# Kernel optimization log

Measured on AMD Instinct MI355X. Metric: run time of the kernel, lower is better.

Reference implementation:

```python
import jax, jax.numpy as jnp
import numpy as np

EPS_NORM = 1e-12   # torch F.normalize eps
GN_EPS = 1e-5      # GroupNorm eps
FACTOR = 5
NUM_HEADS = 8
NEG_SLOPE = 0.01   # LeakyReLU default


def _l2norm(x, axis):
    n = jnp.sqrt(jnp.sum(x * x, axis=axis, keepdims=True))
    return x / jnp.maximum(n, EPS_NORM)


def setup_inputs() -> dict:
    key = jax.random.key(0)
    B, C, H, W, D = 2, 256, 16, 16, 16
    N = H * W * D
    sample_k = FACTOR * int(np.ceil(np.log(N)))  # 45
    ks = jax.random.split(key, 8)
    s = 0.02
    return {
        "x": jax.random.normal(ks[0], (B, C, H, W, D), jnp.float32),
        "W_qkvv": jax.random.normal(ks[1], (C, 4 * C), jnp.float32) * s,
        "W_out": jax.random.normal(ks[2], (C, C), jnp.float32) * s,
        "b_out": jnp.zeros((C,), jnp.float32),
        "W_out2": jax.random.normal(ks[3], (C, C), jnp.float32) * s,
        "b_out2": jnp.zeros((C,), jnp.float32),
        "gamma1": 0.1 * jnp.ones((C,), jnp.float32),
        "conv_w": jax.random.normal(ks[4], (C, C, 3, 3, 3), jnp.float32) * s,
        "gn_w": jnp.ones((C,), jnp.float32),
        "gn_b": jnp.zeros((C,), jnp.float32),
        "index_sample": jax.random.randint(ks[5], (N, sample_k), 0, N),
    }


def reference(x, W_qkvv, W_out, b_out, W_out2, b_out2, gamma1, conv_w, gn_w, gn_b, index_sample):
    B, C, H, Wd, D = x.shape
    N = H * Wd * D
    nh = NUM_HEADS
    dh = C // nh
    xs = x.reshape(B, C, N).transpose(0, 2, 1)                    # [B,N,C]
    qkvv = (xs @ W_qkvv).reshape(B, N, 4, nh, dh).transpose(2, 0, 3, 1, 4)  # [4,B,nh,N,dh]
    q, k, v_ca, v_sa = qkvv[0], qkvv[1], qkvv[2], qkvv[3]
    q = _l2norm(q, axis=-2)   # normalize over sequence dim (dim=-2 in torch)
    k = _l2norm(k, axis=-2)

    u = FACTOR * int(np.ceil(np.log(N)))
    # --- ProbSparse _prob_QK ---
    K_sample = k[:, :, index_sample, :]                            # [B,nh,N,sk,dh]
    QK_sample = jnp.einsum('bhle,bhlse->bhls', q, K_sample)        # [B,nh,N,sk]
    M = QK_sample.max(-1) - QK_sample.sum(-1) / N                  # sparsity measure
    _, M_top = jax.lax.top_k(M, u)                                 # [B,nh,u]
    b_idx = jnp.arange(B)[:, None, None]
    h_idx = jnp.arange(nh)[None, :, None]
    Q_red = q[b_idx, h_idx, M_top]                                 # [B,nh,u,dh]
    scores = jnp.einsum('bhud,bhld->bhul', Q_red, k)               # [B,nh,u,N]

    # --- spatial (ProbSparse) context ---
    ctx = jnp.broadcast_to(v_sa.mean(axis=-2, keepdims=True), v_sa.shape)  # [B,nh,N,dh]
    attn_sa = jax.nn.softmax(scores, axis=-1)
    upd = jnp.einsum('bhul,bhld->bhud', attn_sa, v_sa)             # [B,nh,u,dh]
    ctx = ctx.at[b_idx, h_idx, M_top].set(upd)

    # --- channel attention (on transposed q,k,v: [B,nh,dh,N]) ---
    qt = q.transpose(0, 1, 3, 2)
    kt = k.transpose(0, 1, 3, 2)
    vt = v_ca.transpose(0, 1, 3, 2)
    attn_ca = jax.nn.softmax(jnp.einsum('bhdn,bhen->bhde', qt, kt), axis=-1)  # [B,nh,dh,dh]
    x_ca = jnp.einsum('bhde,bhen->bhdn', attn_ca, vt).transpose(0, 3, 1, 2).reshape(B, N, C)
    x_sa = ctx.transpose(0, 3, 1, 2).reshape(B, N, C)              # matches source permute
    x_sa = x_sa @ W_out + b_out                                    # dead branch (source discards)
    x_ca = x_ca @ W_out2 + b_out2
    epa = x_ca  # source: x = x_SA + x_CA; x = x_CA  -> only CA branch survives

    attn = xs + gamma1 * epa                                       # [B,N,C]
    attn = attn.reshape(B, H, Wd, D, C).transpose(0, 4, 1, 2, 3)   # [B,C,H,W,D]

    # conv8: Dropout3d (eval=id) -> Conv3d(3x3x3, no bias) -> GroupNorm(1 group)
    y = jax.lax.conv_general_dilated(attn, conv_w, (1, 1, 1), [(1, 1)] * 3,
                                     dimension_numbers=('NCDHW', 'OIDHW', 'NCDHW'))
    mu = y.mean(axis=(1, 2, 3, 4), keepdims=True)
    var = y.var(axis=(1, 2, 3, 4), keepdims=True)
    y = (y - mu) / jnp.sqrt(var + GN_EPS)
    y = y * gn_w[None, :, None, None, None] + gn_b[None, :, None, None, None]
    y = y + attn
    return jnp.where(y >= 0, y, NEG_SLOPE * y)
```

## Files before the change

### kernel.cpp

```cpp
#include <hip/hip_runtime.h>
#include <hip/hip_bf16.h>
#include <stdint.h>


#define B_ 2
#define C_ 256
#define N_ 4096
#define NH 8
#define PADV 5832
#define CN  (C_*N_)
#define BCN (B_*CN)

typedef unsigned short u16;
typedef unsigned int   u32;

using frag16 = __attribute__((ext_vector_type(8))) short;
using f32x4  = __attribute__((ext_vector_type(4))) float;

__device__ __forceinline__ u16 f2bf(float f) {
    u32 u = __float_as_uint(f);
    u += 0x7fff + ((u >> 16) & 1);
    return (u16)(u >> 16);
}
__device__ __forceinline__ float bb(u16 h) { return __uint_as_float((u32)h << 16); }
__device__ __forceinline__ void gld16(const void* g, void* l) {
    __builtin_amdgcn_global_load_lds((const __attribute__((address_space(1))) u32*)g,
                                     (__attribute__((address_space(3))) u32*)l, 16, 0, 0);
}
__device__ __forceinline__ int padrow(int n) {
    int z = n >> 8, y = (n >> 4) & 15, x = n & 15;
    return (z + 1) * 324 + (y + 1) * 18 + (x + 1);
}

#define OFF_TB    0
#define OFF_SP    3145728
#define OFF_XCAB  3276800
#define OFF_PK    0
#define OFF_ATTB  6291456
#define OFF_ATTP  7340032
#define OFF_WT2   8833024
#define OFF_W2B   9717760
#define OFF_WQB   9750528
#define OFF_XT    9848832
#define OFF_RED   10897408
 
__global__ __launch_bounds__(256) void k_prep(const float* __restrict__ CW, const float* __restrict__ W2,
                                              const float* __restrict__ Wq, const float* __restrict__ X,
                                              u16* __restrict__ WT2, u16* __restrict__ W2B,
                                              u16* __restrict__ Wqb, u16* __restrict__ XT,
                                              u32* __restrict__ APz) {
    __shared__ float ts[32][33];
    int blk = blockIdx.x, tid = threadIdx.x;
    if (blk < 6912) {
        int o = blk * 256 + tid;
        int ci = o & 255, co = (o >> 8) & 255, t = o >> 16;
        WT2[o] = f2bf(CW[((size_t)co * 256 + ci) * 27 + t]);
    } else if (blk < 6976) {
        int bi = blk - 6912; int c0 = (bi & 7) * 32, p0 = (bi >> 3) * 32;
        int tx = tid & 31, ty = tid >> 5;
#pragma unroll
        for (int i = 0; i < 4; ++i) ts[ty + i * 8][tx] = W2[(size_t)(p0 + ty + i * 8) * 256 + c0 + tx];
        __syncthreads();
#pragma unroll
        for (int i = 0; i < 4; ++i) W2B[(size_t)(c0 + ty + i * 8) * 256 + p0 + tx] = f2bf(ts[tx][ty + i * 8]);
    } else if (blk < 7744) {
        int o = (blk - 6976) * 256 + tid;
        int c = o & 255, j = o >> 8;
        Wqb[o] = f2bf(Wq[(size_t)c * 1024 + j]);
    } else if (blk < 9792) {
        int idx = blk - 7744;
        int n0 = (idx & 127) * 32, c0 = ((idx >> 7) & 7) * 32, b = idx >> 10;
        int tx = tid & 31, ty = tid >> 5;
        const float* Xb = X + (size_t)b * CN;
#pragma unroll
        for (int i = 0; i < 4; ++i) ts[ty + i * 8][tx] = Xb[(size_t)(c0 + ty + i * 8) * N_ + n0 + tx];
        __syncthreads();
        u16* Xo = XT + (size_t)b * N_ * C_;
#pragma unroll
        for (int i = 0; i < 4; ++i) Xo[(size_t)(n0 + ty + i * 8) * C_ + c0 + tx] = f2bf(ts[tx][ty + i * 8]);
    } else {
        APz[(size_t)(blk - 9792) * 256 + tid] = 0;
    }
}

__global__ __launch_bounds__(256) void k_qkv_mfma(const u16* __restrict__ Wqb, const u16* __restrict__ XT,
                                                  u16* __restrict__ Tb) {
    __shared__ __align__(16) u16 As[2][8192], Bs[2][8192];
    int n0 = blockIdx.x * 128, j0 = blockIdx.y * 128, b = blockIdx.z;
    int tid = threadIdx.x, lane = tid & 63, w = tid >> 6;
    int wm = w & 1, wn = w >> 1, qm = lane >> 4, lm = lane & 15;
    int srow = lane >> 3;
    int sperm = (((lane & 7) ^ srow) << 3);
    const u16* aB = Wqb + ((size_t)(j0 + w * 32 + srow) << 8) + sperm;
    const u16* bB = XT + ((size_t)(b * N_ + n0 + w * 32 + srow) << 8) + sperm;
    int rdp = ((lm & 7) << 3);
    f32x4 acc[4][4] = {};
    auto stg = [&](int p, int kc) {
#pragma unroll
        for (int i = 0; i < 4; ++i) {
            gld16(aB + i * 2048 + kc * 64, &As[p][w * 2048 + i * 512]);
            gld16(bB + i * 2048 + kc * 64, &Bs[p][w * 2048 + i * 512]);
        }
    };
    stg(0, 0);
#pragma unroll
    for (int kt = 0; kt < 4; ++kt) {
        int p = kt & 1;
        __syncthreads();
        if (kt < 3) stg(p ^ 1, kt + 1);
#pragma unroll
        for (int c2 = 0; c2 < 2; ++c2) {
            frag16 af[4], bf[4];
#pragma unroll
            for (int i = 0; i < 4; ++i)
                af[i] = *(const frag16*)&As[p][(wm * 64 + i * 16 + lm) * 64 + ((((c2 * 4 + qm) << 3) ^ rdp))];
#pragma unroll
            for (int j = 0; j < 4; ++j)
                bf[j] = *(const frag16*)&Bs[p][(wn * 64 + j * 16 + lm) * 64 + ((((c2 * 4 + qm) << 3) ^ rdp))];
#pragma unroll
            for (int i = 0; i < 4; ++i)
#pragma unroll
                for (int j = 0; j < 4; ++j)
                    acc[i][j] = __builtin_amdgcn_mfma_f32_16x16x32_bf16(af[i], bf[j], acc[i][j], 0, 0, 0);
        }
    }
    u16* To = Tb + ((size_t)b * 768 + j0 + wm * 64) * N_ + n0 + wn * 64;
#pragma unroll
    for (int i = 0; i < 4; ++i)
#pragma unroll
        for (int j = 0; j < 4; ++j)
#pragma unroll
            for (int r = 0; r < 4; ++r)
                To[(size_t)(i * 16 + qm * 4 + r) * N_ + j * 16 + lm] = f2bf(acc[i][j][r]);
}

__global__ __launch_bounds__(256) void k_l2norm(u16* __restrict__ Tb) {
    int bj = blockIdx.x; int b = bj >> 9, j = bj & 511;
    u16* row = Tb + ((size_t)b * 768 + j) * N_;
    float s = 0.f;
    for (int u = threadIdx.x * 8; u < N_; u += 2048) {
        uint4 vv = *(const uint4*)(row + u);
        const u16* h = (const u16*)&vv;
#pragma unroll
        for (int i = 0; i < 8; ++i) { float f = bb(h[i]); s += f * f; }
    }
#pragma unroll
    for (int off = 32; off; off >>= 1) s += __shfl_down(s, off);
    __shared__ float rs_[4]; __shared__ float rtot;
    int lane = threadIdx.x & 63, wv = threadIdx.x >> 6;
    if (!lane) rs_[wv] = s;
    __syncthreads();
    if (threadIdx.x == 0) rtot = 1.0f / fmaxf(sqrtf(rs_[0] + rs_[1] + rs_[2] + rs_[3]), 1e-12f);
    __syncthreads();
    float rn = rtot;
    for (int u = threadIdx.x * 8; u < N_; u += 2048) {
        uint4 vv = *(const uint4*)(row + u);
        u16* h = (u16*)&vv;
#pragma unroll
        for (int i = 0; i < 8; ++i) h[i] = f2bf(bb(h[i]) * rn);
        *(uint4*)(row + u) = vv;
    }
}

__global__ __launch_bounds__(256) void k_ca_part(const u16* __restrict__ Tb, float* __restrict__ SP) {
    int s = blockIdx.x, h = blockIdx.y, b = blockIdx.z;
    int t = threadIdx.x, d = t & 31, eg = t >> 5;
    const u16* Q  = Tb + ((size_t)b * 768 + h * 32 + d) * N_ + s * 512;
    const u16* K0 = Tb + ((size_t)b * 768 + 256 + h * 32 + eg * 4) * N_ + s * 512;
    float a0 = 0.f, a1 = 0.f, a2 = 0.f, a3 = 0.f;
    for (int u = 0; u < 512; u += 8) {
        uint4 qv = *(const uint4*)(Q + u);
        uint4 k0 = *(const uint4*)(K0 + u);
        uint4 k1 = *(const uint4*)(K0 + (size_t)N_ + u);
        uint4 k2 = *(const uint4*)(K0 + (size_t)2 * N_ + u);
        uint4 k3 = *(const uint4*)(K0 + (size_t)3 * N_ + u);
        const u16 *qh = (const u16*)&qv, *h0 = (const u16*)&k0, *h1 = (const u16*)&k1,
                  *h2 = (const u16*)&k2, *h3 = (const u16*)&k3;
#pragma unroll
        for (int i = 0; i < 8; ++i) {
            float qf = bb(qh[i]);
            a0 += qf * bb(h0[i]); a1 += qf * bb(h1[i]);
            a2 += qf * bb(h2[i]); a3 += qf * bb(h3[i]);
        }
    }
    float* o = SP + (((size_t)(b * NH + h)) * 8 + s) * 1024 + d * 32 + eg * 4;
    o[0] = a0; o[1] = a1; o[2] = a2; o[3] = a3;
}

__global__ __launch_bounds__(256) void k_ca_apply(const u16* __restrict__ Tb, const float* __restrict__ SP,
                                                  u16* __restrict__ XCAb) {
    int n0 = blockIdx.x * 256, h = blockIdx.y, b = blockIdx.z;
    __shared__ float raw[1024];
    __shared__ float Ae[32][32];
    int tid = threadIdx.x;
    const float* Sp = SP + ((size_t)(b * NH + h)) * 8192;
    for (int u = tid; u < 1024; u += 256) {
        float v = 0.f;
#pragma unroll
        for (int s = 0; s < 8; ++s) v += Sp[s * 1024 + u];
        raw[u] = v;
    }
    __syncthreads();
    if (tid < 32) {
        float m = -1e30f;
#pragma unroll
        for (int e = 0; e < 32; ++e) m = fmaxf(m, raw[tid * 32 + e]);
        float ex[32]; float sm = 0.f;
#pragma unroll
        for (int e = 0; e < 32; ++e) { ex[e] = __expf(raw[tid * 32 + e] - m); sm += ex[e]; }
        float rinv = 1.0f / sm;
#pragma unroll
        for (int e = 0; e < 32; ++e) Ae[e][tid] = ex[e] * rinv;
    }
    __syncthreads();
    int n = n0 + tid;
    const u16* V = Tb + ((size_t)b * 768 + 512 + h * 32) * N_ + n;
    float acc[32];
#pragma unroll
    for (int d = 0; d < 32; ++d) acc[d] = 0.f;
#pragma unroll
    for (int e = 0; e < 32; ++e) {
        float v = bb(V[(size_t)e * N_]);
#pragma unroll
        for (int dg = 0; dg < 8; ++dg) {
            float4 a4 = *(const float4*)&Ae[e][dg * 4];
            acc[dg * 4 + 0] += a4.x * v; acc[dg * 4 + 1] += a4.y * v;
            acc[dg * 4 + 2] += a4.z * v; acc[dg * 4 + 3] += a4.w * v;
        }
    }
    u16* o = XCAb + ((size_t)b * N_ + n) * C_ + h * 32;
#pragma unroll
    for (int dg = 0; dg < 8; ++dg) {
        ushort4 pk;
        pk.x = f2bf(acc[dg * 4 + 0]); pk.y = f2bf(acc[dg * 4 + 1]);
        pk.z = f2bf(acc[dg * 4 + 2]); pk.w = f2bf(acc[dg * 4 + 3]);
        *(ushort4*)(o + dg * 4) = pk;
    }
}

__global__ __launch_bounds__(256) void k_out2_mfma(const u16* __restrict__ W2B, const u16* __restrict__ XCAb,
                                                   const float* __restrict__ bias2, const float* __restrict__ g1,
                                                   const float* __restrict__ X, u16* __restrict__ ATTb,
                                                   u16* __restrict__ ATTp) {
    __shared__ __align__(16) u16 As[2][8192], Bs[2][8192];
    int n0 = blockIdx.x * 128, c0 = blockIdx.y * 128, b = blockIdx.z;
    int tid = threadIdx.x, lane = tid & 63, w = tid >> 6;
    int wm = w & 1, wn = w >> 1, qm = lane >> 4, lm = lane & 15;
    int srow = lane >> 3;
    int sperm = (((lane & 7) ^ srow) << 3);
    const u16* aB = W2B + ((size_t)(c0 + w * 32 + srow) << 8) + sperm;
    const u16* bB = XCAb + ((size_t)(b * N_ + n0 + w * 32 + srow) << 8) + sperm;
    int rdp = ((lm & 7) << 3);
    f32x4 acc[4][4] = {};
    auto stg = [&](int p, int kc) {
#pragma unroll
        for (int i = 0; i < 4; ++i) {
            gld16(aB + i * 2048 + kc * 64, &As[p][w * 2048 + i * 512]);
            gld16(bB + i * 2048 + kc * 64, &Bs[p][w * 2048 + i * 512]);
        }
    };
    stg(0, 0);
#pragma unroll
    for (int kt = 0; kt < 4; ++kt) {
        int p = kt & 1;
        __syncthreads();
        if (kt < 3) stg(p ^ 1, kt + 1);
#pragma unroll
        for (int c2 = 0; c2 < 2; ++c2) {
            frag16 af[4], bf[4];
#pragma unroll
            for (int i = 0; i < 4; ++i)
                af[i] = *(const frag16*)&As[p][(wm * 64 + i * 16 + lm) * 64 + ((((c2 * 4 + qm) << 3) ^ rdp))];
#pragma unroll
            for (int j = 0; j < 4; ++j)
                bf[j] = *(const frag16*)&Bs[p][(wn * 64 + j * 16 + lm) * 64 + ((((c2 * 4 + qm) << 3) ^ rdp))];
#pragma unroll
            for (int i = 0; i < 4; ++i)
#pragma unroll
                for (int j = 0; j < 4; ++j)
                    acc[i][j] = __builtin_amdgcn_mfma_f32_16x16x32_bf16(af[i], bf[j], acc[i][j], 0, 0, 0);
        }
    }
    int c_base = c0 + wm * 64, n_base = n0 + wn * 64;
    const float* xin = X + (size_t)b * CN;
    u16* Ao = ATTb + (size_t)b * CN;
    u16* Ap = ATTp + ((size_t)b * PADV << 8);
    float val[4][4][4];
#pragma unroll
    for (int i = 0; i < 4; ++i)
#pragma unroll
        for (int r = 0; r < 4; ++r) {
            int c = c_base + i * 16 + qm * 4 + r;
            float gv = g1[c], bi = bias2[c];
#pragma unroll
            for (int j = 0; j < 4; ++j) {
                int n = n_base + j * 16 + lm;
                float v = xin[(size_t)c * N_ + n] + gv * (acc[i][j][r] + bi);
                val[i][j][r] = v;
                Ao[(size_t)c * N_ + n] = f2bf(v);
            }
        }
#pragma unroll
    for (int j = 0; j < 4; ++j) {
        int n = n_base + j * 16 + lm;
        int pr = padrow(n);
#pragma unroll
        for (int i = 0; i < 4; ++i) {
            ushort4 pk;
            pk.x = f2bf(val[i][j][0]); pk.y = f2bf(val[i][j][1]);
            pk.z = f2bf(val[i][j][2]); pk.w = f2bf(val[i][j][3]);
            *(ushort4*)&Ap[((size_t)pr << 8) + c_base + i * 16 + qm * 4] = pk;
        }
    }
}

__global__ __launch_bounds__(256) void k_conv_mfma(const u16* __restrict__ WT2, const u16* __restrict__ ATTp,
                                                   float* __restrict__ Pk) {
    __shared__ __align__(16) u16 As[2][8192], Bs[2][8192];
    int n0 = blockIdx.x * 128;
    int co0 = (blockIdx.y & 1) * 128, ks = blockIdx.y >> 1;
    int b = blockIdx.z;
    int tid = threadIdx.x, lane = tid & 63, w = tid >> 6;
    int wm = w & 1, wn = w >> 1, qm = lane >> 4, lm = lane & 15;
    int srow = lane >> 3;
    int sperm = (((lane & 7) ^ srow) << 3);
    const u16* aB = WT2 + (((size_t)ks * 9 * 256 + co0 + w * 32 + srow) << 8) + sperm;
    int prA[4];
#pragma unroll
    for (int i = 0; i < 4; ++i) prA[i] = padrow(n0 + w * 32 + i * 8 + srow) << 8;
    const u16* bB = ATTp + ((size_t)b * PADV << 8) + ((ks - 1) * 324 << 8) + sperm;
    int rdp = ((lm & 7) << 3);
    f32x4 acc[4][4] = {};
    auto stg = [&](int p, int kt) {
        int tap9 = kt >> 2, kc = kt & 3;
        int K9 = ((tap9 / 3) - 1) * 18 + (tap9 % 3 - 1);
#pragma unroll
        for (int i = 0; i < 4; ++i) {
            gld16(aB + (size_t)tap9 * 65536 + i * 2048 + kc * 64, &As[p][w * 2048 + i * 512]);
            gld16(bB + prA[i] + K9 * 256 + kc * 64,              &Bs[p][w * 2048 + i * 512]);
        }
    };
    stg(0, 0);
#pragma unroll
    for (int kt = 0; kt < 36; ++kt) {
        int p = kt & 1;
        __syncthreads();
        if (kt < 35) stg(p ^ 1, kt + 1);
#pragma unroll
        for (int c2 = 0; c2 < 2; ++c2) {
            frag16 af[4], bf[4];
#pragma unroll
            for (int i = 0; i < 4; ++i)
                af[i] = *(const frag16*)&As[p][(wm * 64 + i * 16 + lm) * 64 + ((((c2 * 4 + qm) << 3) ^ rdp))];
#pragma unroll
            for (int j = 0; j < 4; ++j)
                bf[j] = *(const frag16*)&Bs[p][(wn * 64 + j * 16 + lm) * 64 + ((((c2 * 4 + qm) << 3) ^ rdp))];
#pragma unroll
            for (int i = 0; i < 4; ++i)
#pragma unroll
                for (int j = 0; j < 4; ++j)
                    acc[i][j] = __builtin_amdgcn_mfma_f32_16x16x32_bf16(af[i], bf[j], acc[i][j], 0, 0, 0);
        }
    }
    float* Pb = Pk + ((size_t)(ks * B_ + b) * C_ + co0 + wm * 64) * N_ + n0 + wn * 64;
#pragma unroll
    for (int i = 0; i < 4; ++i)
#pragma unroll
        for (int j = 0; j < 4; ++j)
#pragma unroll
            for (int r = 0; r < 4; ++r)
                Pb[(size_t)(i * 16 + qm * 4 + r) * N_ + j * 16 + lm] = acc[i][j][r];
}

__global__ __launch_bounds__(256) void k_gn_reduce(float* __restrict__ Pk, float* __restrict__ RED) {
    int blk = blockIdx.x, b = blockIdx.y;
    size_t base = (size_t)b * CN + (size_t)blk * 16384;
    float* p0 = Pk + base;
    const float* p1 = Pk + BCN + base;
    const float* p2 = Pk + (size_t)2 * BCN + base;
    float s = 0.f, q = 0.f;
    for (int u = threadIdx.x * 4; u < 16384; u += 1024) {
        float4 a = *(const float4*)&p0[u];
        float4 c1 = *(const float4*)&p1[u];
        float4 c2 = *(const float4*)&p2[u];
        a.x += c1.x + c2.x; a.y += c1.y + c2.y; a.z += c1.z + c2.z; a.w += c1.w + c2.w;
        *(float4*)&p0[u] = a;
        s += a.x + a.y + a.z + a.w;
        q += a.x * a.x + a.y * a.y + a.z * a.z + a.w * a.w;
    }
#pragma unroll
    for (int off = 32; off; off >>= 1) { s += __shfl_down(s, off); q += __shfl_down(q, off); }
    __shared__ float rs_[4], rq[4];
    int lane = threadIdx.x & 63, wv = threadIdx.x >> 6;
    if (!lane) { rs_[wv] = s; rq[wv] = q; }
    __syncthreads();
    if (threadIdx.x == 0) {
        RED[((size_t)b * 64 + blk) * 2 + 0] = rs_[0] + rs_[1] + rs_[2] + rs_[3];
        RED[((size_t)b * 64 + blk) * 2 + 1] = rq[0] + rq[1] + rq[2] + rq[3];
    }
}

__global__ __launch_bounds__(256) void k_final(const float* __restrict__ Y, const u16* __restrict__ ATTb,
                                               const float* __restrict__ RED, const float* __restrict__ gw,
                                               const float* __restrict__ gb, float* __restrict__ out) {
    int i = blockIdx.x * 256 + threadIdx.x;
    int b = i >> 20;
    int c = (i >> 12) & 255;
    __shared__ float smu[2];
    if (threadIdx.x < 64) {
        float s = RED[((size_t)b * 64 + threadIdx.x) * 2 + 0];
        float q = RED[((size_t)b * 64 + threadIdx.x) * 2 + 1];
#pragma unroll
        for (int off = 32; off; off >>= 1) { s += __shfl_down(s, off); q += __shfl_down(q, off); }
        if (threadIdx.x == 0) {
            float inv = 1.0f / (float)CN;
            float mu = s * inv, var = q * inv - mu * mu;
            smu[0] = mu; smu[1] = rsqrtf(var + 1e-5f);
        }
    }
    __syncthreads();
    float v = (Y[i] - smu[0]) * smu[1] * gw[c] + gb[c] + bb(ATTb[i]);
    out[i] = v >= 0.f ? v : 0.01f * v;
}

extern "C" void kernel_launch(void* const* d_in, const int* in_sizes, int n_in,
                              void* d_out, int out_size, void* d_ws, size_t ws_size,
                              hipStream_t stream) {
    const float* x      = (const float*)d_in[0];
    const float* Wqkvv  = (const float*)d_in[1];
    const float* W_out2 = (const float*)d_in[4];
    const float* b_out2 = (const float*)d_in[5];
    const float* gamma1 = (const float*)d_in[6];
    const float* conv_w = (const float*)d_in[7];
    const float* gn_w   = (const float*)d_in[8];
    const float* gn_b   = (const float*)d_in[9];
    float* out = (float*)d_out;
    float* ws = (float*)d_ws;

    u16*   Tb   = (u16*)(ws + OFF_TB);
    float* SP   = ws + OFF_SP;
    u16*   XCAb = (u16*)(ws + OFF_XCAB);
    float* Pk   = ws + OFF_PK;
    float* Y    = Pk;
    u16*   ATTb = (u16*)(ws + OFF_ATTB);
    u16*   ATTp = (u16*)(ws + OFF_ATTP);
    u16*   WT2  = (u16*)(ws + OFF_WT2);
    u16*   W2B  = (u16*)(ws + OFF_W2B);
    u16*   Wqb  = (u16*)(ws + OFF_WQB);
    u16*   XT   = (u16*)(ws + OFF_XT);
    float* RED  = ws + OFF_RED;

    k_prep      <<<15624, 256, 0, stream>>>(conv_w, W_out2, Wqkvv, x, WT2, W2B, Wqb, XT, (u32*)ATTp);
    k_qkv_mfma  <<<dim3(N_ / 128, 6, B_), 256, 0, stream>>>(Wqb, XT, Tb);
    k_l2norm    <<<B_ * 512, 256, 0, stream>>>(Tb);
    k_ca_part   <<<dim3(8, NH, B_), 256, 0, stream>>>(Tb, SP);
    k_ca_apply  <<<dim3(N_ / 256, NH, B_), 256, 0, stream>>>(Tb, SP, XCAb);
    k_out2_mfma <<<dim3(N_ / 128, C_ / 128, B_), 256, 0, stream>>>(W2B, XCAb, b_out2, gamma1, x, ATTb, ATTp);
    k_conv_mfma <<<dim3(N_ / 128, 6, B_), 256, 0, stream>>>(WT2, ATTp, Pk);
    k_gn_reduce <<<dim3(64, B_), 256, 0, stream>>>(Pk, RED);
    k_final     <<<(B_ * CN) / 256, 256, 0, stream>>>(Y, ATTb, RED, gn_w, gn_b, out);
}
```

Before: 191.4 us.

## Fuse L2 norm into QKV GEMM, bf16 conv partials, coalesce weight prep

The separate L2-norm kernel is removed. The QKV GEMM epilogue now accumulates per-row sums of squares into a buffer with atomics, and the cross-attention softmax applies the inverse norms to the raw Q·K scores. The conv split-K partials and the reduced output are stored as bf16 instead of fp32, which halves that memory traffic at some cost in precision. Weight preparation uses coalesced LDS-staged transposes instead of strided scalar gathers, and the CA partial kernel is split into 32 sequence chunks for more parallelism.

```diff
diff --git a/kernel.cpp b/kernel.cpp
--- a/kernel.cpp
+++ b/kernel.cpp
@@ -34,41 +34,52 @@
 
 #define OFF_TB    0
 #define OFF_SP    3145728
-#define OFF_XCAB  3276800
-#define OFF_PK    0
+#define OFF_XCAB  3670016
+#define OFF_PKB   0
+#define OFF_Y     3145728
 #define OFF_ATTB  6291456
 #define OFF_ATTP  7340032
 #define OFF_WT2   8833024
 #define OFF_W2B   9717760
 #define OFF_WQB   9750528
 #define OFF_XT    9848832
-#define OFF_RED   10897408
- 
+#define OFF_RSQ   10897408
+#define OFF_RED   10898432
+
 __global__ __launch_bounds__(256) void k_prep(const float* __restrict__ CW, const float* __restrict__ W2,
                                               const float* __restrict__ Wq, const float* __restrict__ X,
                                               u16* __restrict__ WT2, u16* __restrict__ W2B,
                                               u16* __restrict__ Wqb, u16* __restrict__ XT,
-                                              u32* __restrict__ APz) {
-    __shared__ float ts[32][33];
+                                              u32* __restrict__ APz, float* __restrict__ RSQ) {
+    __shared__ __align__(16) float ls[6912];
+    float (*ts)[33] = (float(*)[33])ls;
     int blk = blockIdx.x, tid = threadIdx.x;
-    if (blk < 6912) {
-        int o = blk * 256 + tid;
-        int ci = o & 255, co = (o >> 8) & 255, t = o >> 16;
-        WT2[o] = f2bf(CW[((size_t)co * 256 + ci) * 27 + t]);
-    } else if (blk < 6976) {
-        int bi = blk - 6912; int c0 = (bi & 7) * 32, p0 = (bi >> 3) * 32;
+    if (blk < 256) {
+        int co = blk;
+        const float* src = CW + (size_t)co * 6912;
+        for (int u = tid; u < 6912; u += 256) ls[u] = src[u];
+        __syncthreads();
+#pragma unroll
+        for (int t = 0; t < 27; ++t)
+            WT2[(((size_t)t * 256 + co) << 8) + tid] = f2bf(ls[tid * 27 + t]);
+    } else if (blk < 320) {
+        int bi = blk - 256; int c0 = (bi & 7) * 32, p0 = (bi >> 3) * 32;
         int tx = tid & 31, ty = tid >> 5;
 #pragma unroll
         for (int i = 0; i < 4; ++i) ts[ty + i * 8][tx] = W2[(size_t)(p0 + ty + i * 8) * 256 + c0 + tx];
         __syncthreads();
 #pragma unroll
         for (int i = 0; i < 4; ++i) W2B[(size_t)(c0 + ty + i * 8) * 256 + p0 + tx] = f2bf(ts[tx][ty + i * 8]);
-    } else if (blk < 7744) {
-        int o = (blk - 6976) * 256 + tid;
-        int c = o & 255, j = o >> 8;
-        Wqb[o] = f2bf(Wq[(size_t)c * 1024 + j]);
-    } else if (blk < 9792) {
-        int idx = blk - 7744;
+    } else if (blk < 512) {
+        int bi = blk - 320; int c0 = (bi & 7) * 32, j0 = (bi >> 3) * 32;
+        int tx = tid & 31, ty = tid >> 5;
+#pragma unroll
+        for (int i = 0; i < 4; ++i) ts[ty + i * 8][tx] = Wq[(size_t)(c0 + ty + i * 8) * 1024 + j0 + tx];
+        __syncthreads();
+#pragma unroll
+        for (int i = 0; i < 4; ++i) Wqb[(size_t)(j0 + ty + i * 8) * 256 + c0 + tx] = f2bf(ts[tx][ty + i * 8]);
+    } else if (blk < 2560) {
+        int idx = blk - 512;
         int n0 = (idx & 127) * 32, c0 = ((idx >> 7) & 7) * 32, b = idx >> 10;
         int tx = tid & 31, ty = tid >> 5;
         const float* Xb = X + (size_t)b * CN;
@@ -78,13 +89,15 @@
         u16* Xo = XT + (size_t)b * N_ * C_;
 #pragma unroll
         for (int i = 0; i < 4; ++i) Xo[(size_t)(n0 + ty + i * 8) * C_ + c0 + tx] = f2bf(ts[tx][ty + i * 8]);
+    } else if (blk < 8392) {
+        APz[(size_t)(blk - 2560) * 256 + tid] = 0;
     } else {
-        APz[(size_t)(blk - 9792) * 256 + tid] = 0;
+        ((float4*)RSQ)[tid] = make_float4(0.f, 0.f, 0.f, 0.f);
     }
 }
 
 __global__ __launch_bounds__(256) void k_qkv_mfma(const u16* __restrict__ Wqb, const u16* __restrict__ XT,
-                                                  u16* __restrict__ Tb) {
+                                                  u16* __restrict__ Tb, float* __restrict__ RSQ) {
     __shared__ __align__(16) u16 As[2][8192], Bs[2][8192];
     int n0 = blockIdx.x * 128, j0 = blockIdx.y * 128, b = blockIdx.z;
     int tid = threadIdx.x, lane = tid & 63, w = tid >> 6;
@@ -132,43 +145,29 @@
 #pragma unroll
             for (int r = 0; r < 4; ++r)
                 To[(size_t)(i * 16 + qm * 4 + r) * N_ + j * 16 + lm] = f2bf(acc[i][j][r]);
-}
-
-__global__ __launch_bounds__(256) void k_l2norm(u16* __restrict__ Tb) {
-    int bj = blockIdx.x; int b = bj >> 9, j = bj & 511;
-    u16* row = Tb + ((size_t)b * 768 + j) * N_;
-    float s = 0.f;
-    for (int u = threadIdx.x * 8; u < N_; u += 2048) {
-        uint4 vv = *(const uint4*)(row + u);
-        const u16* h = (const u16*)&vv;
-#pragma unroll
-        for (int i = 0; i < 8; ++i) { float f = bb(h[i]); s += f * f; }
-    }
-#pragma unroll
-    for (int off = 32; off; off >>= 1) s += __shfl_down(s, off);
-    __shared__ float rs_[4]; __shared__ float rtot;
-    int lane = threadIdx.x & 63, wv = threadIdx.x >> 6;
-    if (!lane) rs_[wv] = s;
-    __syncthreads();
-    if (threadIdx.x == 0) rtot = 1.0f / fmaxf(sqrtf(rs_[0] + rs_[1] + rs_[2] + rs_[3]), 1e-12f);
-    __syncthreads();
-    float rn = rtot;
-    for (int u = threadIdx.x * 8; u < N_; u += 2048) {
-        uint4 vv = *(const uint4*)(row + u);
-        u16* h = (u16*)&vv;
-#pragma unroll
-        for (int i = 0; i < 8; ++i) h[i] = f2bf(bb(h[i]) * rn);
-        *(uint4*)(row + u) = vv;
+    if (j0 < 512) {
+#pragma unroll
+        for (int i = 0; i < 4; ++i)
+#pragma unroll
+            for (int r = 0; r < 4; ++r) {
+                float s = 0.f;
+#pragma unroll
+                for (int j = 0; j < 4; ++j) s += acc[i][j][r] * acc[i][j][r];
+                s += __shfl_xor(s, 1); s += __shfl_xor(s, 2);
+                s += __shfl_xor(s, 4); s += __shfl_xor(s, 8);
+                if (lm == 0)
+                    atomicAdd(&RSQ[b * 512 + j0 + wm * 64 + i * 16 + qm * 4 + r], s);
+            }
     }
 }
 
 __global__ __launch_bounds__(256) void k_ca_part(const u16* __restrict__ Tb, float* __restrict__ SP) {
     int s = blockIdx.x, h = blockIdx.y, b = blockIdx.z;
     int t = threadIdx.x, d = t & 31, eg = t >> 5;
-    const u16* Q  = Tb + ((size_t)b * 768 + h * 32 + d) * N_ + s * 512;
-    const u16* K0 = Tb + ((size_t)b * 768 + 256 + h * 32 + eg * 4) * N_ + s * 512;
+    const u16* Q  = Tb + ((size_t)b * 768 + h * 32 + d) * N_ + s * 128;
+    const u16* K0 = Tb + ((size_t)b * 768 + 256 + h * 32 + eg * 4) * N_ + s * 128;
     float a0 = 0.f, a1 = 0.f, a2 = 0.f, a3 = 0.f;
-    for (int u = 0; u < 512; u += 8) {
+    for (int u = 0; u < 128; u += 8) {
         uint4 qv = *(const uint4*)(Q + u);
         uint4 k0 = *(const uint4*)(K0 + u);
         uint4 k1 = *(const uint4*)(K0 + (size_t)N_ + u);
@@ -183,34 +182,40 @@
             a2 += qf * bb(h2[i]); a3 += qf * bb(h3[i]);
         }
     }
-    float* o = SP + (((size_t)(b * NH + h)) * 8 + s) * 1024 + d * 32 + eg * 4;
+    float* o = SP + (((size_t)(b * NH + h)) * 32 + s) * 1024 + d * 32 + eg * 4;
     o[0] = a0; o[1] = a1; o[2] = a2; o[3] = a3;
 }
 
 __global__ __launch_bounds__(256) void k_ca_apply(const u16* __restrict__ Tb, const float* __restrict__ SP,
-                                                  u16* __restrict__ XCAb) {
+                                                  const float* __restrict__ RSQ, u16* __restrict__ XCAb) {
     int n0 = blockIdx.x * 256, h = blockIdx.y, b = blockIdx.z;
     __shared__ float raw[1024];
     __shared__ float Ae[32][32];
+    __shared__ float sq[32], sk[32];
     int tid = threadIdx.x;
-    const float* Sp = SP + ((size_t)(b * NH + h)) * 8192;
+    const float* Sp = SP + ((size_t)(b * NH + h)) * 32768;
     for (int u = tid; u < 1024; u += 256) {
         float v = 0.f;
 #pragma unroll
-        for (int s = 0; s < 8; ++s) v += Sp[s * 1024 + u];
+        for (int s = 0; s < 32; ++s) v += Sp[s * 1024 + u];
         raw[u] = v;
+    }
+    if (tid < 32) {
+        sq[tid] = 1.0f / fmaxf(sqrtf(RSQ[b * 512 + h * 32 + tid]), 1e-12f);
+        sk[tid] = 1.0f / fmaxf(sqrtf(RSQ[b * 512 + 256 + h * 32 + tid]), 1e-12f);
     }
     __syncthreads();
     if (tid < 32) {
-        float m = -1e30f;
-#pragma unroll
-        for (int e = 0; e < 32; ++e) m = fmaxf(m, raw[tid * 32 + e]);
-        float ex[32]; float sm = 0.f;
-#pragma unroll
-        for (int e = 0; e < 32; ++e) { ex[e] = __expf(raw[tid * 32 + e] - m); sm += ex[e]; }
+        float iq = sq[tid];
+        float sv[32]; float m = -1e30f;
+#pragma unroll
+        for (int e = 0; e < 32; ++e) { sv[e] = raw[tid * 32 + e] * iq * sk[e]; m = fmaxf(m, sv[e]); }
+        float sm = 0.f;
+#pragma unroll
+        for (int e = 0; e < 32; ++e) { sv[e] = __expf(sv[e] - m); sm += sv[e]; }
         float rinv = 1.0f / sm;
 #pragma unroll
-        for (int e = 0; e < 32; ++e) Ae[e][tid] = ex[e] * rinv;
+        for (int e = 0; e < 32; ++e) Ae[e][tid] = sv[e] * rinv;
     }
     __syncthreads();
     int n = n0 + tid;
@@ -315,7 +320,7 @@
 }
 
 __global__ __launch_bounds__(256) void k_conv_mfma(const u16* __restrict__ WT2, const u16* __restrict__ ATTp,
-                                                   float* __restrict__ Pk) {
+                                                   u16* __restrict__ Pk) {
     __shared__ __align__(16) u16 As[2][8192], Bs[2][8192];
     int n0 = blockIdx.x * 128;
     int co0 = (blockIdx.y & 1) * 128, ks = blockIdx.y >> 1;
@@ -362,31 +367,38 @@
                     acc[i][j] = __builtin_amdgcn_mfma_f32_16x16x32_bf16(af[i], bf[j], acc[i][j], 0, 0, 0);
         }
     }
-    float* Pb = Pk + ((size_t)(ks * B_ + b) * C_ + co0 + wm * 64) * N_ + n0 + wn * 64;
+    u16* Pb = Pk + ((size_t)(ks * B_ + b) * C_ + co0 + wm * 64) * N_ + n0 + wn * 64;
 #pragma unroll
     for (int i = 0; i < 4; ++i)
 #pragma unroll
         for (int j = 0; j < 4; ++j)
 #pragma unroll
             for (int r = 0; r < 4; ++r)
-                Pb[(size_t)(i * 16 + qm * 4 + r) * N_ + j * 16 + lm] = acc[i][j][r];
-}
-
-__global__ __launch_bounds__(256) void k_gn_reduce(float* __restrict__ Pk, float* __restrict__ RED) {
+                Pb[(size_t)(i * 16 + qm * 4 + r) * N_ + j * 16 + lm] = f2bf(acc[i][j][r]);
+}
+
+__global__ __launch_bounds__(256) void k_gn_reduce(const u16* __restrict__ Pk, u16* __restrict__ Y,
+                                                   float* __restrict__ RED) {
     int blk = blockIdx.x, b = blockIdx.y;
     size_t base = (size_t)b * CN + (size_t)blk * 16384;
-    float* p0 = Pk + base;
-    const float* p1 = Pk + BCN + base;
-    const float* p2 = Pk + (size_t)2 * BCN + base;
+    const u16* p0 = Pk + base;
+    const u16* p1 = Pk + BCN + base;
+    const u16* p2 = Pk + (size_t)2 * BCN + base;
+    u16* y = Y + base;
     float s = 0.f, q = 0.f;
-    for (int u = threadIdx.x * 4; u < 16384; u += 1024) {
-        float4 a = *(const float4*)&p0[u];
-        float4 c1 = *(const float4*)&p1[u];
-        float4 c2 = *(const float4*)&p2[u];
-        a.x += c1.x + c2.x; a.y += c1.y + c2.y; a.z += c1.z + c2.z; a.w += c1.w + c2.w;
-        *(float4*)&p0[u] = a;
-        s += a.x + a.y + a.z + a.w;
-        q += a.x * a.x + a.y * a.y + a.z * a.z + a.w * a.w;
+    for (int u = threadIdx.x * 8; u < 16384; u += 2048) {
+        uint4 a = *(const uint4*)&p0[u];
+        uint4 c1 = *(const uint4*)&p1[u];
+        uint4 c2 = *(const uint4*)&p2[u];
+        const u16 *A = (const u16*)&a, *B1 = (const u16*)&c1, *C2 = (const u16*)&c2;
+        __align__(16) u16 outp[8];
+#pragma unroll
+        for (int i = 0; i < 8; ++i) {
+            float v = bb(A[i]) + bb(B1[i]) + bb(C2[i]);
+            s += v; q += v * v;
+            outp[i] = f2bf(v);
+        }
+        *(uint4*)&y[u] = *(const uint4*)outp;
     }
 #pragma unroll
     for (int off = 32; off; off >>= 1) { s += __shfl_down(s, off); q += __shfl_down(q, off); }
@@ -400,7 +412,7 @@
     }
 }
 
-__global__ __launch_bounds__(256) void k_final(const float* __restrict__ Y, const u16* __restrict__ ATTb,
+__global__ __launch_bounds__(256) void k_final(const u16* __restrict__ Y, const u16* __restrict__ ATTb,
                                                const float* __restrict__ RED, const float* __restrict__ gw,
                                                const float* __restrict__ gb, float* __restrict__ out) {
     int i = blockIdx.x * 256 + threadIdx.x;
@@ -419,7 +431,7 @@
         }
     }
     __syncthreads();
-    float v = (Y[i] - smu[0]) * smu[1] * gw[c] + gb[c] + bb(ATTb[i]);
+    float v = (bb(Y[i]) - smu[0]) * smu[1] * gw[c] + gb[c] + bb(ATTb[i]);
     out[i] = v >= 0.f ? v : 0.01f * v;
 }
 
@@ -440,23 +452,23 @@
     u16*   Tb   = (u16*)(ws + OFF_TB);
     float* SP   = ws + OFF_SP;
     u16*   XCAb = (u16*)(ws + OFF_XCAB);
-    float* Pk   = ws + OFF_PK;
-    float* Y    = Pk;
+    u16*   Pk   = (u16*)(ws + OFF_PKB);
+    u16*   Y    = (u16*)(ws + OFF_Y);
     u16*   ATTb = (u16*)(ws + OFF_ATTB);
     u16*   ATTp = (u16*)(ws + OFF_ATTP);
     u16*   WT2  = (u16*)(ws + OFF_WT2);
     u16*   W2B  = (u16*)(ws + OFF_W2B);
     u16*   Wqb  = (u16*)(ws + OFF_WQB);
     u16*   XT   = (u16*)(ws + OFF_XT);
+    float* RSQ  = ws + OFF_RSQ;
     float* RED  = ws + OFF_RED;
 
-    k_prep      <<<15624, 256, 0, stream>>>(conv_w, W_out2, Wqkvv, x, WT2, W2B, Wqb, XT, (u32*)ATTp);
-    k_qkv_mfma  <<<dim3(N_ / 128, 6, B_), 256, 0, stream>>>(Wqb, XT, Tb);
-    k_l2norm    <<<B_ * 512, 256, 0, stream>>>(Tb);
-    k_ca_part   <<<dim3(8, NH, B_), 256, 0, stream>>>(Tb, SP);
-    k_ca_apply  <<<dim3(N_ / 256, NH, B_), 256, 0, stream>>>(Tb, SP, XCAb);
+    k_prep      <<<8393, 256, 0, stream>>>(conv_w, W_out2, Wqkvv, x, WT2, W2B, Wqb, XT, (u32*)ATTp, RSQ);
+    k_qkv_mfma  <<<dim3(N_ / 128, 6, B_), 256, 0, stream>>>(Wqb, XT, Tb, RSQ);
+    k_ca_part   <<<dim3(32, NH, B_), 256, 0, stream>>>(Tb, SP);
+    k_ca_apply  <<<dim3(N_ / 256, NH, B_), 256, 0, stream>>>(Tb, SP, RSQ, XCAb);
     k_out2_mfma <<<dim3(N_ / 128, C_ / 128, B_), 256, 0, stream>>>(W2B, XCAb, b_out2, gamma1, x, ATTb, ATTp);
     k_conv_mfma <<<dim3(N_ / 128, 6, B_), 256, 0, stream>>>(WT2, ATTp, Pk);
-    k_gn_reduce <<<dim3(64, B_), 256, 0, stream>>>(Pk, RED);
+    k_gn_reduce <<<dim3(64, B_), 256, 0, stream>>>(Pk, Y, RED);
     k_final     <<<(B_ * CN) / 256, 256, 0, stream>>>(Y, ATTb, RED, gn_w, gn_b, out);
 }
```

Result: faster. 181.2 us (-5.3%).
